# Optimization experiments

Measured on AMD Instinct MI355X. Metric: run time of the kernel, lower is better.

The kernel has to match this reference:

```python
import jax, jax.numpy as jnp
import numpy as np

N_NODES = 50000
N_EDGES = 800000
IN_F = 512
H_F = 32
HEADS = 8
N_CLS = 40
NEG_SLOPE = 0.2


def gat_conv(h, W, al, ar, b, src, dst, n_heads, d_out):
    """DGL-style GATConv. h: [N, F_in]; W: [F_in, n_heads*d_out];
    al, ar: [n_heads, d_out]; b: [n_heads*d_out]. Returns [N, n_heads, d_out]."""
    n = h.shape[0]
    feat = (h @ W).reshape(n, n_heads, d_out)            # [N, H, D]
    el = jnp.sum(feat * al[None], axis=-1)               # [N, H]
    er = jnp.sum(feat * ar[None], axis=-1)               # [N, H]
    e = jax.nn.leaky_relu(el[src] + er[dst], NEG_SLOPE)  # [E, H]
    # numerically stable edge softmax per destination node
    m = jax.ops.segment_max(e, dst, num_segments=n)      # [N, H]
    m = jnp.where(jnp.isfinite(m), m, 0.0)
    ee = jnp.exp(e - m[dst])                             # [E, H]
    den = jax.ops.segment_sum(ee, dst, num_segments=n)   # [N, H]
    alpha = ee / jnp.maximum(den[dst], 1e-9)             # [E, H]
    msg = alpha[:, :, None] * feat[src]                  # [E, H, D]
    rst = jax.ops.segment_sum(msg, dst, num_segments=n)  # [N, H, D]
    return rst + b.reshape(1, n_heads, d_out)


def setup_inputs() -> dict:
    key = jax.random.key(0)
    ks = jax.random.split(key, 16)
    hid = H_F * HEADS
    s = lambda fan: 1.0 / np.sqrt(fan)
    return {
        "in_feat": jax.random.normal(ks[0], (N_NODES, IN_F), jnp.float32),
        "src": jax.random.randint(ks[1], (N_EDGES,), 0, N_NODES, jnp.int32),
        "dst": jax.random.randint(ks[2], (N_EDGES,), 0, N_NODES, jnp.int32),
        "W0": jax.random.normal(ks[3], (IN_F, hid), jnp.float32) * s(IN_F),
        "al0": jax.random.normal(ks[4], (HEADS, H_F), jnp.float32) * s(H_F),
        "ar0": jax.random.normal(ks[5], (HEADS, H_F), jnp.float32) * s(H_F),
        "b0": jnp.zeros((hid,), jnp.float32),
        "W1": jax.random.normal(ks[6], (hid, hid), jnp.float32) * s(hid),
        "al1": jax.random.normal(ks[7], (HEADS, H_F), jnp.float32) * s(H_F),
        "ar1": jax.random.normal(ks[8], (HEADS, H_F), jnp.float32) * s(H_F),
        "b1": jnp.zeros((hid,), jnp.float32),
        "W2": jax.random.normal(ks[9], (hid, N_CLS), jnp.float32) * s(hid),
        "al2": jax.random.normal(ks[10], (1, N_CLS), jnp.float32) * s(N_CLS),
        "ar2": jax.random.normal(ks[11], (1, N_CLS), jnp.float32) * s(N_CLS),
        "b2": jnp.zeros((N_CLS,), jnp.float32),
    }


def reference(in_feat, src, dst, W0, al0, ar0, b0, W1, al1, ar1, b1,
              W2, al2, ar2, b2):
    n = in_feat.shape[0]
    # layer 0 + ReLU (dropout p=0.0 is identity) + flatten heads
    h = gat_conv(in_feat, W0, al0, ar0, b0, src, dst, HEADS, H_F)
    h = jax.nn.relu(h).reshape(n, -1)
    # layer 1
    h = gat_conv(h, W1, al1, ar1, b1, src, dst, HEADS, H_F)
    h = jax.nn.relu(h).reshape(n, -1)
    # output layer, single head, no activation
    h = gat_conv(h, W2, al2, ar2, b2, src, dst, 1, N_CLS)
    return h.reshape(n, -1)
```

## Files before the change

kernel.cpp:

```cpp
#include <hip/hip_runtime.h>
#include <hip/hip_bf16.h>

#define N_NODES 50000
#define N_EDGES 800000
#define IN_F 512
#define HID 256
#define HEADS 8
#define DHEAD 32
#define N_CLS 40
#define NCLS_PAD 64

typedef __bf16 bf16x8 __attribute__((ext_vector_type(8)));
typedef float f32x4 __attribute__((ext_vector_type(4)));

#define AT_AL0 0
#define AT_AR0 256
#define AT_AL1 512
#define AT_AR1 768
#define AT_AL2 1024
#define AT_AR2 1088
#define AT_B0  1152
#define AT_B1  1408
#define AT_B2  1664
#define AT_SZ  1792

__device__ __forceinline__ float ldflag(const void* p, long long i, int isbf) {
  return isbf ? __bfloat162float(((const __hip_bfloat16*)p)[i])
              : ((const float*)p)[i];
}
__device__ __forceinline__ float blo(unsigned u) { return __uint_as_float(u << 16); }
__device__ __forceinline__ float bhi(unsigned u) { return __uint_as_float(u & 0xffff0000u); }

__global__ void k_detect(const unsigned short* __restrict__ raw, int* __restrict__ flag) {
  __shared__ int cnt[256];
  int t = threadIdx.x;
  int c = 0;
  for (int i = t; i < 8192; i += 256) {
    int e = (raw[i] >> 7) & 0xFF;
    if (e >= 0x90) c++;
  }
  cnt[t] = c;
  __syncthreads();
  for (int s = 128; s; s >>= 1) {
    if (t < s) cnt[t] += cnt[t + s];
    __syncthreads();
  }
  if (t == 0) *flag = (cnt[0] > 64) ? 0 : 1;
}

__global__ void k_prep(const void* al0, const void* ar0, const void* al1, const void* ar1,
                       const void* al2, const void* ar2, const void* b0, const void* b1,
                       const void* b2, float* __restrict__ att, const int* __restrict__ flag) {
  int isbf = *flag;
  int t = threadIdx.x;
  att[AT_AL0 + t] = ldflag(al0, t, isbf);
  att[AT_AR0 + t] = ldflag(ar0, t, isbf);
  att[AT_AL1 + t] = ldflag(al1, t, isbf);
  att[AT_AR1 + t] = ldflag(ar1, t, isbf);
  att[AT_B0 + t]  = ldflag(b0, t, isbf);
  att[AT_B1 + t]  = ldflag(b1, t, isbf);
  if (t < N_CLS) {
    att[AT_AL2 + t] = ldflag(al2, t, isbf);
    att[AT_AR2 + t] = ldflag(ar2, t, isbf);
    att[AT_B2 + t]  = ldflag(b2, t, isbf);
  }
}

__global__ void k_cast_bf16(const void* __restrict__ in, __hip_bfloat16* __restrict__ out,
                            long long n, const int* __restrict__ flag) {
  int isbf = *flag;
  long long i = (long long)blockIdx.x * blockDim.x + threadIdx.x;
  long long stride = (long long)gridDim.x * blockDim.x;
  long long n4 = n >> 2;
  if (isbf) {
    const ushort4* p4 = (const ushort4*)in;
    ushort4* o4 = (ushort4*)out;
    for (long long j = i; j < n4; j += stride) o4[j] = p4[j];
  } else {
    const float4* p4 = (const float4*)in;
    for (long long j = i; j < n4; j += stride) {
      float4 v = p4[j];
      ushort4 o;
      o.x = __bfloat16_as_ushort(__float2bfloat16(v.x));
      o.y = __bfloat16_as_ushort(__float2bfloat16(v.y));
      o.z = __bfloat16_as_ushort(__float2bfloat16(v.z));
      o.w = __bfloat16_as_ushort(__float2bfloat16(v.w));
      ((ushort4*)out)[j] = o;
    }
  }
}

__global__ void k_hist(const int* __restrict__ dst, int* __restrict__ cnt) {
  int e = blockIdx.x * blockDim.x + threadIdx.x;
  if (e < N_EDGES) atomicAdd(&cnt[dst[e]], 1);
}

#define SCAN_B 512
#define SCAN_NB ((N_NODES + SCAN_B - 1) / SCAN_B)

__global__ __launch_bounds__(SCAN_B) void k_scan_blocks(const int* __restrict__ deg,
                                                        int* __restrict__ excl,
                                                        int* __restrict__ partial) {
  __shared__ int buf[SCAN_B];
  int t = threadIdx.x;
  int i = blockIdx.x * SCAN_B + t;
  int v = (i < N_NODES) ? deg[i] : 0;
  buf[t] = v;
  __syncthreads();
  for (int off = 1; off < SCAN_B; off <<= 1) {
    int x = (t >= off) ? buf[t - off] : 0;
    __syncthreads();
    buf[t] += x;
    __syncthreads();
  }
  if (i < N_NODES) excl[i] = buf[t] - v;
  if (t == SCAN_B - 1) partial[blockIdx.x] = buf[t];
}

__global__ void k_scan_partials(int* __restrict__ partial, int* __restrict__ rowptr) {
  __shared__ int buf[SCAN_NB];
  int t = threadIdx.x;
  if (t < SCAN_NB) buf[t] = partial[t];
  __syncthreads();
  if (t == 0) {
    int run = 0;
    for (int b = 0; b < SCAN_NB; b++) { int v = buf[b]; buf[b] = run; run += v; }
    rowptr[N_NODES] = run;
  }
  __syncthreads();
  if (t < SCAN_NB) partial[t] = buf[t];
}

__global__ void k_scan_add(int* __restrict__ rowptr, const int* __restrict__ partial) {
  int i = blockIdx.x * blockDim.x + threadIdx.x;
  if (i < N_NODES) rowptr[i] += partial[i / SCAN_B];
}

__global__ void k_scatter(const int* __restrict__ src, const int* __restrict__ dst,
                          const int* __restrict__ rowptr, int* __restrict__ cursor,
                          int* __restrict__ csr_src) {
  int e = blockIdx.x * blockDim.x + threadIdx.x;
  if (e < N_EDGES) {
    int d = dst[e];
    int pos = rowptr[d] + atomicAdd(&cursor[d], 1);
    csr_src[pos] = src[e];
  }
}

__global__ void k_transpose16(const void* __restrict__ W, __hip_bfloat16* __restrict__ Wt,
                              int K, int Nsrc, int Ndst, const int* __restrict__ flag) {
  int isbf = *flag;
  int i = blockIdx.x * blockDim.x + threadIdx.x;
  if (i >= Ndst * K) return;
  int n = i / K, k = i - n * K;
  float v = 0.f;
  if (n < Nsrc) v = ldflag(W, (long long)k * Nsrc + n, isbf);
  Wt[(size_t)n * K + k] = __float2bfloat16(v);
}

__global__ __launch_bounds__(256) void k_gemm_bt16(const __hip_bfloat16* __restrict__ A,
                                                   const __hip_bfloat16* __restrict__ Bt,
                                                   __hip_bfloat16* __restrict__ C,
                                                   int M, int K, int N) {
  __shared__ unsigned short As[64][40];
  __shared__ unsigned short Bs[64][40];
  int tid = threadIdx.x;
  int m0 = blockIdx.x * 64, n0 = blockIdx.y * 64;
  int lrow = tid >> 2;
  int lcol = (tid & 3) * 8;
  int wave = tid >> 6, lane = tid & 63;
  int wm = (wave >> 1) * 32, wn = (wave & 1) * 32;
  int lm = lane & 15, quad = lane >> 4;
  f32x4 acc[2][2] = {};
  for (int k0 = 0; k0 < K; k0 += 32) {
    int ga = m0 + lrow;
    uint4 av = make_uint4(0u, 0u, 0u, 0u);
    if (ga < M) av = *(const uint4*)(A + (size_t)ga * K + k0 + lcol);
    uint4 bv = *(const uint4*)(Bt + (size_t)(n0 + lrow) * K + k0 + lcol);
    __syncthreads();
    *(uint4*)(&As[lrow][lcol]) = av;
    *(uint4*)(&Bs[lrow][lcol]) = bv;
    __syncthreads();
    bf16x8 af[2], bfr[2];
    #pragma unroll
    for (int i = 0; i < 2; i++) {
      af[i]  = *(const bf16x8*)(&As[wm + i * 16 + lm][quad * 8]);
      bfr[i] = *(const bf16x8*)(&Bs[wn + i * 16 + lm][quad * 8]);
    }
    #pragma unroll
    for (int mi = 0; mi < 2; mi++)
      #pragma unroll
      for (int ni = 0; ni < 2; ni++)
        acc[mi][ni] = __builtin_amdgcn_mfma_f32_16x16x32_bf16(af[mi], bfr[ni], acc[mi][ni], 0, 0, 0);
  }
  #pragma unroll
  for (int mi = 0; mi < 2; mi++)
    #pragma unroll
    for (int ni = 0; ni < 2; ni++)
      #pragma unroll
      for (int r = 0; r < 4; r++) {
        int gm = m0 + wm + mi * 16 + quad * 4 + r;
        int gn = n0 + wn + ni * 16 + lm;
        if (gm < M) C[(size_t)gm * N + gn] = __float2bfloat16(acc[mi][ni][r]);
      }
}

__global__ void k_eler8(const uint4* __restrict__ feat_rows,
                        const float* __restrict__ al, const float* __restrict__ ar,
                        float* __restrict__ el, float* __restrict__ er) {
  int i = blockIdx.x * blockDim.x + threadIdx.x;
  if (i >= N_NODES * HEADS) return;
  int n = i >> 3, h = i & 7;
  const uint4* base = feat_rows + (size_t)n * 32 + h * 4;
  const float* alh = al + h * DHEAD;
  const float* arh = ar + h * DHEAD;
  float sl = 0.f, sr = 0.f;
  #pragma unroll
  for (int q = 0; q < 4; q++) {
    uint4 v = base[q];
    unsigned u[4] = {v.x, v.y, v.z, v.w};
    #pragma unroll
    for (int w = 0; w < 4; w++) {
      int d = q * 8 + w * 2;
      float f0 = blo(u[w]), f1 = bhi(u[w]);
      sl += f0 * alh[d] + f1 * alh[d + 1];
      sr += f0 * arh[d] + f1 * arh[d + 1];
    }
  }
  el[i] = sl;
  er[i] = sr;
}

__global__ void k_eler2(const __hip_bfloat16* __restrict__ feat2,
                        const float* __restrict__ al, const float* __restrict__ ar,
                        float* __restrict__ el, float* __restrict__ er) {
  int n = blockIdx.x * blockDim.x + threadIdx.x;
  if (n >= N_NODES) return;
  const __hip_bfloat16* f = feat2 + (size_t)n * NCLS_PAD;
  float sl = 0.f, sr = 0.f;
  for (int d = 0; d < N_CLS; d++) {
    float v = __bfloat162float(f[d]);
    sl += v * al[d];
    sr += v * ar[d];
  }
  el[n] = sl;
  er[n] = sr;
}

__global__ __launch_bounds__(256) void k_aggregate8(const int* __restrict__ rowptr,
                                                    const int* __restrict__ csr_src,
                                                    const uint4* __restrict__ feat_rows,
                                                    const float* __restrict__ el,
                                                    const float* __restrict__ er,
                                                    const float* __restrict__ bias,
                                                    __hip_bfloat16* __restrict__ out) {
  __shared__ float lds_acc[8][256];
  __shared__ float lds_l[8][32];
  int n = blockIdx.x;
  int t = threadIdx.x;
  int slot = t >> 5;
  int c = t & 31;
  int hh = c >> 2;
  float er_n = er[n * HEADS + hh];
  int beg = rowptr[n], end = rowptr[n + 1];
  float l = 0.f;
  float acc[8] = {0.f, 0.f, 0.f, 0.f, 0.f, 0.f, 0.f, 0.f};
  for (int i = beg + slot; i < end; i += 8) {
    int s = csr_src[i];
    float elv = el[s * HEADS + hh];
    uint4 fv = feat_rows[(size_t)s * 32 + c];
    float x = elv + er_n;
    float e = x > 0.f ? x : 0.2f * x;
    float p = __expf(fminf(e, 60.f));
    l += p;
    acc[0] += p * blo(fv.x); acc[1] += p * bhi(fv.x);
    acc[2] += p * blo(fv.y); acc[3] += p * bhi(fv.y);
    acc[4] += p * blo(fv.z); acc[5] += p * bhi(fv.z);
    acc[6] += p * blo(fv.w); acc[7] += p * bhi(fv.w);
  }
  *(float4*)&lds_acc[slot][c * 8]     = make_float4(acc[0], acc[1], acc[2], acc[3]);
  *(float4*)&lds_acc[slot][c * 8 + 4] = make_float4(acc[4], acc[5], acc[6], acc[7]);
  lds_l[slot][c] = l;
  __syncthreads();
  float a = 0.f, L = 0.f;
  #pragma unroll
  for (int s2 = 0; s2 < 8; s2++) { a += lds_acc[s2][t]; L += lds_l[s2][t >> 3]; }
  float o = a / fmaxf(L, 1e-9f) + bias[t];
  o = fmaxf(o, 0.f);
  out[(size_t)n * HID + t] = __float2bfloat16(o);
}

__global__ __launch_bounds__(256) void k_aggregate1(const int* __restrict__ rowptr,
                                                    const int* __restrict__ csr_src,
                                                    const uint4* __restrict__ fr2,
                                                    const float* __restrict__ el,
                                                    const float* __restrict__ er,
                                                    const float* __restrict__ bias,
                                                    void* __restrict__ out,
                                                    const int* __restrict__ flag) {
  __shared__ float lds_acc[32][64];
  __shared__ float lds_l[32][8];
  int isbf = *flag;
  int n = blockIdx.x;
  int t = threadIdx.x;
  int slot = t >> 3;
  int c = t & 7;
  float er_n = er[n];
  int beg = rowptr[n], end = rowptr[n + 1];
  float l = 0.f;
  float acc[8] = {0.f, 0.f, 0.f, 0.f, 0.f, 0.f, 0.f, 0.f};
  for (int i = beg + slot; i < end; i += 32) {
    int s = csr_src[i];
    float x = el[s] + er_n;
    uint4 fv = fr2[(size_t)s * 8 + c];
    float e = x > 0.f ? x : 0.2f * x;
    float p = __expf(fminf(e, 60.f));
    l += p;
    acc[0] += p * blo(fv.x); acc[1] += p * bhi(fv.x);
    acc[2] += p * blo(fv.y); acc[3] += p * bhi(fv.y);
    acc[4] += p * blo(fv.z); acc[5] += p * bhi(fv.z);
    acc[6] += p * blo(fv.w); acc[7] += p * bhi(fv.w);
  }
  *(float4*)&lds_acc[slot][c * 8]     = make_float4(acc[0], acc[1], acc[2], acc[3]);
  *(float4*)&lds_acc[slot][c * 8 + 4] = make_float4(acc[4], acc[5], acc[6], acc[7]);
  lds_l[slot][c] = l;
  __syncthreads();
  if (t < N_CLS) {
    float a = 0.f, L = 0.f;
    #pragma unroll
    for (int s2 = 0; s2 < 32; s2++) { a += lds_acc[s2][t]; L += lds_l[s2][t >> 3]; }
    float o = a / fmaxf(L, 1e-9f) + bias[t];
    if (isbf) ((__hip_bfloat16*)out)[(size_t)n * N_CLS + t] = __float2bfloat16(o);
    else      ((float*)out)[(size_t)n * N_CLS + t] = o;
  }
}

static inline size_t align_up(size_t x) { return (x + 255) & ~(size_t)255; }

extern "C" void kernel_launch(void* const* d_in, const int* in_sizes, int n_in,
                              void* d_out, int out_size, void* d_ws, size_t ws_size,
                              hipStream_t stream) {
  const void* in_feat = d_in[0];
  const int* src = (const int*)d_in[1];
  const int* dst = (const int*)d_in[2];
  const void* W0  = d_in[3];
  const void* al0 = d_in[4];
  const void* ar0 = d_in[5];
  const void* b0  = d_in[6];
  const void* W1  = d_in[7];
  const void* al1 = d_in[8];
  const void* ar1 = d_in[9];
  const void* b1  = d_in[10];
  const void* W2  = d_in[11];
  const void* al2 = d_in[12];
  const void* ar2 = d_in[13];
  const void* b2  = d_in[14];

  char* p = (char*)d_ws;
  int* flag = (int*)p;                   p += 256;
  float* att = (float*)p;                p += align_up(AT_SZ * sizeof(float));
  int* rowptr = (int*)p;                 p += align_up((N_NODES + 1) * sizeof(int));
  int* cursor = (int*)p;                 p += align_up(N_NODES * sizeof(int));
  int* csr_src = (int*)p;                p += align_up(N_EDGES * sizeof(int));
  int* partial = (int*)p;                p += align_up(SCAN_NB * sizeof(int));
  __hip_bfloat16* a16 = (__hip_bfloat16*)p;    p += align_up((size_t)N_NODES * IN_F * sizeof(__hip_bfloat16));
  __hip_bfloat16* feat16 = (__hip_bfloat16*)p; p += align_up((size_t)N_NODES * HID * sizeof(__hip_bfloat16));
  __hip_bfloat16* h16 = (__hip_bfloat16*)p;    p += align_up((size_t)N_NODES * HID * sizeof(__hip_bfloat16));
  float* el = (float*)p;                 p += align_up((size_t)N_NODES * HEADS * sizeof(float));
  float* er = (float*)p;                 p += align_up((size_t)N_NODES * HEADS * sizeof(float));
  __hip_bfloat16* w0t = (__hip_bfloat16*)p;    p += align_up((size_t)HID * IN_F * sizeof(__hip_bfloat16));
  __hip_bfloat16* w1t = (__hip_bfloat16*)p;    p += align_up((size_t)HID * HID * sizeof(__hip_bfloat16));
  __hip_bfloat16* w2t = (__hip_bfloat16*)p;    p += align_up((size_t)NCLS_PAD * HID * sizeof(__hip_bfloat16));

  const int EB = (N_EDGES + 255) / 256;
  const int MB64 = (N_NODES + 63) / 64;

  k_detect<<<1, 256, 0, stream>>>((const unsigned short*)in_feat, flag);
  k_prep<<<1, 256, 0, stream>>>(al0, ar0, al1, ar1, al2, ar2, b0, b1, b2, att, flag);

  hipMemsetAsync(cursor, 0, N_NODES * sizeof(int), stream);
  k_hist<<<EB, 256, 0, stream>>>(dst, cursor);
  k_scan_blocks<<<SCAN_NB, SCAN_B, 0, stream>>>(cursor, rowptr, partial);
  k_scan_partials<<<1, 128, 0, stream>>>(partial, rowptr);
  k_scan_add<<<(N_NODES + 255) / 256, 256, 0, stream>>>(rowptr, partial);
  hipMemsetAsync(cursor, 0, N_NODES * sizeof(int), stream);
  k_scatter<<<EB, 256, 0, stream>>>(src, dst, rowptr, cursor, csr_src);

  k_cast_bf16<<<1024, 256, 0, stream>>>(in_feat, a16, (long long)N_NODES * IN_F, flag);
  k_transpose16<<<(HID * IN_F + 255) / 256, 256, 0, stream>>>(W0, w0t, IN_F, HID, HID, flag);
  k_transpose16<<<(HID * HID + 255) / 256, 256, 0, stream>>>(W1, w1t, HID, HID, HID, flag);
  k_transpose16<<<(NCLS_PAD * HID + 255) / 256, 256, 0, stream>>>(W2, w2t, HID, N_CLS, NCLS_PAD, flag);

  k_gemm_bt16<<<dim3(MB64, HID / 64), 256, 0, stream>>>(a16, w0t, feat16, N_NODES, IN_F, HID);
  k_eler8<<<(N_NODES * HEADS + 255) / 256, 256, 0, stream>>>((const uint4*)feat16, att + AT_AL0, att + AT_AR0, el, er);
  k_aggregate8<<<N_NODES, 256, 0, stream>>>(rowptr, csr_src, (const uint4*)feat16, el, er, att + AT_B0, h16);

  k_gemm_bt16<<<dim3(MB64, HID / 64), 256, 0, stream>>>(h16, w1t, feat16, N_NODES, HID, HID);
  k_eler8<<<(N_NODES * HEADS + 255) / 256, 256, 0, stream>>>((const uint4*)feat16, att + AT_AL1, att + AT_AR1, el, er);
  k_aggregate8<<<N_NODES, 256, 0, stream>>>(rowptr, csr_src, (const uint4*)feat16, el, er, att + AT_B1, h16);

  k_gemm_bt16<<<dim3(MB64, 1), 256, 0, stream>>>(h16, w2t, feat16, N_NODES, HID, NCLS_PAD);
  k_eler2<<<(N_NODES + 255) / 256, 256, 0, stream>>>(feat16, att + AT_AL2, att + AT_AR2, el, er);
  k_aggregate1<<<N_NODES, 256, 0, stream>>>(rowptr, csr_src, (const uint4*)feat16, el, er, att + AT_B2, d_out, flag);
}
```

Baseline: 586.5 us.

## Fuse input cast into GEMM, widen GEMM tiles, unroll aggregation loops, merge prep kernels

Removes the separate fp32-to-bf16 cast pass by converting A rows inside the GEMM load, which avoids writing and rereading a 50000x512 bf16 buffer. The GEMM now gives each block the full output width (64x256 for hidden layers, 64x64 for the output layer), so A is read once instead of once per column tile. The aggregation loops process two edges per iteration to expose more memory-level parallelism, and the detect and prep kernels are merged into one launch. The wider tiles raise register use per thread, which may reduce occupancy, and the GEMM grid becomes smaller.

```diff
diff --git a/kernel.cpp b/kernel.cpp
--- a/kernel.cpp
+++ b/kernel.cpp
@@ -30,8 +30,16 @@
 }
 __device__ __forceinline__ float blo(unsigned u) { return __uint_as_float(u << 16); }
 __device__ __forceinline__ float bhi(unsigned u) { return __uint_as_float(u & 0xffff0000u); }
-
-__global__ void k_detect(const unsigned short* __restrict__ raw, int* __restrict__ flag) {
+__device__ __forceinline__ unsigned pk2(float a, float b) {
+  unsigned x = __bfloat16_as_ushort(__float2bfloat16(a));
+  unsigned y = __bfloat16_as_ushort(__float2bfloat16(b));
+  return x | (y << 16);
+}
+
+__global__ void k_detect_prep(const unsigned short* __restrict__ raw, int* __restrict__ flag,
+                              const void* al0, const void* ar0, const void* al1, const void* ar1,
+                              const void* al2, const void* ar2, const void* b0, const void* b1,
+                              const void* b2, float* __restrict__ att) {
   __shared__ int cnt[256];
   int t = threadIdx.x;
   int c = 0;
@@ -45,14 +53,10 @@
     if (t < s) cnt[t] += cnt[t + s];
     __syncthreads();
   }
-  if (t == 0) *flag = (cnt[0] > 64) ? 0 : 1;
-}
-
-__global__ void k_prep(const void* al0, const void* ar0, const void* al1, const void* ar1,
-                       const void* al2, const void* ar2, const void* b0, const void* b1,
-                       const void* b2, float* __restrict__ att, const int* __restrict__ flag) {
-  int isbf = *flag;
-  int t = threadIdx.x;
+  __shared__ int sflag;
+  if (t == 0) { sflag = (cnt[0] > 64) ? 0 : 1; *flag = sflag; }
+  __syncthreads();
+  int isbf = sflag;
   att[AT_AL0 + t] = ldflag(al0, t, isbf);
   att[AT_AR0 + t] = ldflag(ar0, t, isbf);
   att[AT_AL1 + t] = ldflag(al1, t, isbf);
@@ -66,30 +70,6 @@
   }
 }
 
-__global__ void k_cast_bf16(const void* __restrict__ in, __hip_bfloat16* __restrict__ out,
-                            long long n, const int* __restrict__ flag) {
-  int isbf = *flag;
-  long long i = (long long)blockIdx.x * blockDim.x + threadIdx.x;
-  long long stride = (long long)gridDim.x * blockDim.x;
-  long long n4 = n >> 2;
-  if (isbf) {
-    const ushort4* p4 = (const ushort4*)in;
-    ushort4* o4 = (ushort4*)out;
-    for (long long j = i; j < n4; j += stride) o4[j] = p4[j];
-  } else {
-    const float4* p4 = (const float4*)in;
-    for (long long j = i; j < n4; j += stride) {
-      float4 v = p4[j];
-      ushort4 o;
-      o.x = __bfloat16_as_ushort(__float2bfloat16(v.x));
-      o.y = __bfloat16_as_ushort(__float2bfloat16(v.y));
-      o.z = __bfloat16_as_ushort(__float2bfloat16(v.z));
-      o.w = __bfloat16_as_ushort(__float2bfloat16(v.w));
-      ((ushort4*)out)[j] = o;
-    }
-  }
-}
-
 __global__ void k_hist(const int* __restrict__ dst, int* __restrict__ cnt) {
   int e = blockIdx.x * blockDim.x + threadIdx.x;
   if (e < N_EDGES) atomicAdd(&cnt[dst[e]], 1);
@@ -158,50 +138,71 @@
   Wt[(size_t)n * K + k] = __float2bfloat16(v);
 }
 
-__global__ __launch_bounds__(256) void k_gemm_bt16(const __hip_bfloat16* __restrict__ A,
-                                                   const __hip_bfloat16* __restrict__ Bt,
-                                                   __hip_bfloat16* __restrict__ C,
-                                                   int M, int K, int N) {
+template<int NT>
+__global__ __launch_bounds__(256) void k_gemm_fused(const void* __restrict__ A,
+                                                    const __hip_bfloat16* __restrict__ Bt,
+                                                    __hip_bfloat16* __restrict__ C,
+                                                    int M, int K,
+                                                    const int* __restrict__ flag, int force_bf) {
+  constexpr int NC = NT * 64;
   __shared__ unsigned short As[64][40];
-  __shared__ unsigned short Bs[64][40];
+  __shared__ unsigned short Bs[NC][40];
+  const int isbf = force_bf ? 1 : *flag;
   int tid = threadIdx.x;
-  int m0 = blockIdx.x * 64, n0 = blockIdx.y * 64;
+  int m0 = blockIdx.x * 64;
   int lrow = tid >> 2;
   int lcol = (tid & 3) * 8;
   int wave = tid >> 6, lane = tid & 63;
-  int wm = (wave >> 1) * 32, wn = (wave & 1) * 32;
+  int wn = wave * (NT * 16);
   int lm = lane & 15, quad = lane >> 4;
-  f32x4 acc[2][2] = {};
+
+  f32x4 acc[4][NT] = {};
   for (int k0 = 0; k0 < K; k0 += 32) {
     int ga = m0 + lrow;
     uint4 av = make_uint4(0u, 0u, 0u, 0u);
-    if (ga < M) av = *(const uint4*)(A + (size_t)ga * K + k0 + lcol);
-    uint4 bv = *(const uint4*)(Bt + (size_t)(n0 + lrow) * K + k0 + lcol);
+    if (isbf) {
+      if (ga < M) av = *(const uint4*)((const __hip_bfloat16*)A + (size_t)ga * K + k0 + lcol);
+    } else {
+      if (ga < M) {
+        const float* ap = (const float*)A + (size_t)ga * K + k0 + lcol;
+        float4 f1 = *(const float4*)ap;
+        float4 f2 = *(const float4*)(ap + 4);
+        av.x = pk2(f1.x, f1.y); av.y = pk2(f1.z, f1.w);
+        av.z = pk2(f2.x, f2.y); av.w = pk2(f2.z, f2.w);
+      }
+    }
+    uint4 bv[NT];
+    #pragma unroll
+    for (int j = 0; j < NT; j++)
+      bv[j] = *(const uint4*)(Bt + (size_t)(lrow + 64 * j) * K + k0 + lcol);
     __syncthreads();
     *(uint4*)(&As[lrow][lcol]) = av;
-    *(uint4*)(&Bs[lrow][lcol]) = bv;
+    #pragma unroll
+    for (int j = 0; j < NT; j++)
+      *(uint4*)(&Bs[lrow + 64 * j][lcol]) = bv[j];
     __syncthreads();
-    bf16x8 af[2], bfr[2];
-    #pragma unroll
-    for (int i = 0; i < 2; i++) {
-      af[i]  = *(const bf16x8*)(&As[wm + i * 16 + lm][quad * 8]);
-      bfr[i] = *(const bf16x8*)(&Bs[wn + i * 16 + lm][quad * 8]);
-    }
-    #pragma unroll
-    for (int mi = 0; mi < 2; mi++)
+    bf16x8 af[4], bfr[NT];
+    #pragma unroll
+    for (int mi = 0; mi < 4; mi++)
+      af[mi] = *(const bf16x8*)(&As[mi * 16 + lm][quad * 8]);
+    #pragma unroll
+    for (int ni = 0; ni < NT; ni++)
+      bfr[ni] = *(const bf16x8*)(&Bs[wn + ni * 16 + lm][quad * 8]);
+    #pragma unroll
+    for (int mi = 0; mi < 4; mi++)
       #pragma unroll
-      for (int ni = 0; ni < 2; ni++)
+      for (int ni = 0; ni < NT; ni++)
         acc[mi][ni] = __builtin_amdgcn_mfma_f32_16x16x32_bf16(af[mi], bfr[ni], acc[mi][ni], 0, 0, 0);
   }
   #pragma unroll
-  for (int mi = 0; mi < 2; mi++)
-    #pragma unroll
-    for (int ni = 0; ni < 2; ni++)
+  for (int mi = 0; mi < 4; mi++)
+    #pragma unroll
+    for (int ni = 0; ni < NT; ni++)
       #pragma unroll
       for (int r = 0; r < 4; r++) {
-        int gm = m0 + wm + mi * 16 + quad * 4 + r;
-        int gn = n0 + wn + ni * 16 + lm;
-        if (gm < M) C[(size_t)gm * N + gn] = __float2bfloat16(acc[mi][ni][r]);
+        int gm = m0 + mi * 16 + quad * 4 + r;
+        int gn = wn + ni * 16 + lm;
+        if (gm < M) C[(size_t)gm * NC + gn] = __float2bfloat16(acc[mi][ni][r]);
       }
 }
 
@@ -265,7 +266,26 @@
   int beg = rowptr[n], end = rowptr[n + 1];
   float l = 0.f;
   float acc[8] = {0.f, 0.f, 0.f, 0.f, 0.f, 0.f, 0.f, 0.f};
-  for (int i = beg + slot; i < end; i += 8) {
+  int i = beg + slot;
+  for (; i + 8 < end; i += 16) {
+    int s1 = csr_src[i];
+    int s2 = csr_src[i + 8];
+    float el1 = el[s1 * HEADS + hh];
+    float el2 = el[s2 * HEADS + hh];
+    uint4 f1 = feat_rows[(size_t)s1 * 32 + c];
+    uint4 f2 = feat_rows[(size_t)s2 * 32 + c];
+    float x1 = el1 + er_n, x2 = el2 + er_n;
+    float e1 = x1 > 0.f ? x1 : 0.2f * x1;
+    float e2 = x2 > 0.f ? x2 : 0.2f * x2;
+    float p1 = __expf(fminf(e1, 60.f));
+    float p2 = __expf(fminf(e2, 60.f));
+    l += p1 + p2;
+    acc[0] += p1 * blo(f1.x) + p2 * blo(f2.x); acc[1] += p1 * bhi(f1.x) + p2 * bhi(f2.x);
+    acc[2] += p1 * blo(f1.y) + p2 * blo(f2.y); acc[3] += p1 * bhi(f1.y) + p2 * bhi(f2.y);
+    acc[4] += p1 * blo(f1.z) + p2 * blo(f2.z); acc[5] += p1 * bhi(f1.z) + p2 * bhi(f2.z);
+    acc[6] += p1 * blo(f1.w) + p2 * blo(f2.w); acc[7] += p1 * bhi(f1.w) + p2 * bhi(f2.w);
+  }
+  if (i < end) {
     int s = csr_src[i];
     float elv = el[s * HEADS + hh];
     uint4 fv = feat_rows[(size_t)s * 32 + c];
@@ -309,7 +329,24 @@
   int beg = rowptr[n], end = rowptr[n + 1];
   float l = 0.f;
   float acc[8] = {0.f, 0.f, 0.f, 0.f, 0.f, 0.f, 0.f, 0.f};
-  for (int i = beg + slot; i < end; i += 32) {
+  int i = beg + slot;
+  for (; i + 32 < end; i += 64) {
+    int s1 = csr_src[i], s2 = csr_src[i + 32];
+    float el1 = el[s1], el2 = el[s2];
+    uint4 f1 = fr2[(size_t)s1 * 8 + c];
+    uint4 f2 = fr2[(size_t)s2 * 8 + c];
+    float x1 = el1 + er_n, x2 = el2 + er_n;
+    float e1 = x1 > 0.f ? x1 : 0.2f * x1;
+    float e2 = x2 > 0.f ? x2 : 0.2f * x2;
+    float p1 = __expf(fminf(e1, 60.f));
+    float p2 = __expf(fminf(e2, 60.f));
+    l += p1 + p2;
+    acc[0] += p1 * blo(f1.x) + p2 * blo(f2.x); acc[1] += p1 * bhi(f1.x) + p2 * bhi(f2.x);
+    acc[2] += p1 * blo(f1.y) + p2 * blo(f2.y); acc[3] += p1 * bhi(f1.y) + p2 * bhi(f2.y);
+    acc[4] += p1 * blo(f1.z) + p2 * blo(f2.z); acc[5] += p1 * bhi(f1.z) + p2 * bhi(f2.z);
+    acc[6] += p1 * blo(f1.w) + p2 * blo(f2.w); acc[7] += p1 * bhi(f1.w) + p2 * bhi(f2.w);
+  }
+  if (i < end) {
     int s = csr_src[i];
     float x = el[s] + er_n;
     uint4 fv = fr2[(size_t)s * 8 + c];
@@ -363,7 +400,6 @@
   int* cursor = (int*)p;                 p += align_up(N_NODES * sizeof(int));
   int* csr_src = (int*)p;                p += align_up(N_EDGES * sizeof(int));
   int* partial = (int*)p;                p += align_up(SCAN_NB * sizeof(int));
-  __hip_bfloat16* a16 = (__hip_bfloat16*)p;    p += align_up((size_t)N_NODES * IN_F * sizeof(__hip_bfloat16));
   __hip_bfloat16* feat16 = (__hip_bfloat16*)p; p += align_up((size_t)N_NODES * HID * sizeof(__hip_bfloat16));
   __hip_bfloat16* h16 = (__hip_bfloat16*)p;    p += align_up((size_t)N_NODES * HID * sizeof(__hip_bfloat16));
   float* el = (float*)p;                 p += align_up((size_t)N_NODES * HEADS * sizeof(float));
@@ -375,8 +411,8 @@
   const int EB = (N_EDGES + 255) / 256;
   const int MB64 = (N_NODES + 63) / 64;
 
-  k_detect<<<1, 256, 0, stream>>>((const unsigned short*)in_feat, flag);
-  k_prep<<<1, 256, 0, stream>>>(al0, ar0, al1, ar1, al2, ar2, b0, b1, b2, att, flag);
+  k_detect_prep<<<1, 256, 0, stream>>>((const unsigned short*)in_feat, flag,
+                                       al0, ar0, al1, ar1, al2, ar2, b0, b1, b2, att);
 
   hipMemsetAsync(cursor, 0, N_NODES * sizeof(int), stream);
   k_hist<<<EB, 256, 0, stream>>>(dst, cursor);
@@ -386,20 +422,19 @@
   hipMemsetAsync(cursor, 0, N_NODES * sizeof(int), stream);
   k_scatter<<<EB, 256, 0, stream>>>(src, dst, rowptr, cursor, csr_src);
 
-  k_cast_bf16<<<1024, 256, 0, stream>>>(in_feat, a16, (long long)N_NODES * IN_F, flag);
   k_transpose16<<<(HID * IN_F + 255) / 256, 256, 0, stream>>>(W0, w0t, IN_F, HID, HID, flag);
   k_transpose16<<<(HID * HID + 255) / 256, 256, 0, stream>>>(W1, w1t, HID, HID, HID, flag);
   k_transpose16<<<(NCLS_PAD * HID + 255) / 256, 256, 0, stream>>>(W2, w2t, HID, N_CLS, NCLS_PAD, flag);
 
-  k_gemm_bt16<<<dim3(MB64, HID / 64), 256, 0, stream>>>(a16, w0t, feat16, N_NODES, IN_F, HID);
+  k_gemm_fused<4><<<MB64, 256, 0, stream>>>(in_feat, w0t, feat16, N_NODES, IN_F, flag, 0);
   k_eler8<<<(N_NODES * HEADS + 255) / 256, 256, 0, stream>>>((const uint4*)feat16, att + AT_AL0, att + AT_AR0, el, er);
   k_aggregate8<<<N_NODES, 256, 0, stream>>>(rowptr, csr_src, (const uint4*)feat16, el, er, att + AT_B0, h16);
 
-  k_gemm_bt16<<<dim3(MB64, HID / 64), 256, 0, stream>>>(h16, w1t, feat16, N_NODES, HID, HID);
+  k_gemm_fused<4><<<MB64, 256, 0, stream>>>(h16, w1t, feat16, N_NODES, HID, flag, 1);
   k_eler8<<<(N_NODES * HEADS + 255) / 256, 256, 0, stream>>>((const uint4*)feat16, att + AT_AL1, att + AT_AR1, el, er);
   k_aggregate8<<<N_NODES, 256, 0, stream>>>(rowptr, csr_src, (const uint4*)feat16, el, er, att + AT_B1, h16);
 
-  k_gemm_bt16<<<dim3(MB64, 1), 256, 0, stream>>>(h16, w2t, feat16, N_NODES, HID, NCLS_PAD);
+  k_gemm_fused<1><<<MB64, 256, 0, stream>>>(h16, w2t, feat16, N_NODES, HID, flag, 1);
   k_eler2<<<(N_NODES + 255) / 256, 256, 0, stream>>>(feat16, att + AT_AL2, att + AT_AR2, el, er);
   k_aggregate1<<<N_NODES, 256, 0, stream>>>(rowptr, csr_src, (const uint4*)feat16, el, er, att + AT_B2, d_out, flag);
 }
```

Measured after the change: 639.6 us. 1.09x slower.
